# Optimization experiments

Measured on AMD Instinct MI355X. Metric: run time of the kernel, lower is better.

Reference implementation:

```python
import jax, jax.numpy as jnp
import numpy as np

N = 100000   # nodes
E = 640000   # edges
H = 8        # attention heads
C = 16       # hidden_channels (per-head out dim)
IN = 4       # in_channels
G = 64       # graphs in the batch
NE = 2       # num_experts
HC = H * C   # 128 = concat feature width
SLOPE = 0.2  # GATConv leaky_relu negative slope


def _p(k, shape):
    return 0.1 * jax.random.normal(k, shape, jnp.float32)


def setup_inputs() -> dict:
    key = jax.random.key(0)
    ks = jax.random.split(key, 32)
    inp = {
        "x": jax.random.normal(ks[0], (N, IN), jnp.float32),
        "edge_index": jax.random.randint(ks[1], (2, E), 0, N),
        "edge_attr": jax.random.normal(ks[2], (E, 1), jnp.float32),
        "batch": jnp.sort(jax.random.randint(ks[3], (N,), 0, G)),
    }
    i = 4
    for l, d in zip((1, 2, 3), (IN, HC, HC)):
        inp[f"w{l}"] = _p(ks[i], (d, HC)); i += 1      # node lin
        inp[f"as{l}"] = _p(ks[i], (H, C)); i += 1      # att_src
        inp[f"ad{l}"] = _p(ks[i], (H, C)); i += 1      # att_dst
        inp[f"we{l}"] = _p(ks[i], (1, HC)); i += 1     # lin_edge
        inp[f"ae{l}"] = _p(ks[i], (H, C)); i += 1      # att_edge
        inp[f"b{l}"] = jnp.zeros((HC,), jnp.float32)
    inp["fw1"] = _p(ks[i], (HC, 4 * C)); inp["fb1"] = jnp.zeros((4 * C,), jnp.float32)
    inp["fw2"] = _p(ks[i + 1], (4 * C, NE)); inp["fb2"] = jnp.zeros((NE,), jnp.float32)
    return inp


def gat_layer(x, src, dst, eattr, w, a_s, a_d, we, a_e, b):
    """PyG GATConv (concat=True, edge_dim=1): gather-attend-segment_softmax-scatter."""
    n = x.shape[0]
    h = (x @ w).reshape(n, H, C)                       # [N,H,C]
    alpha_src = jnp.sum(h * a_s, axis=-1)              # [N,H]
    alpha_dst = jnp.sum(h * a_d, axis=-1)              # [N,H]
    ef = (eattr @ we).reshape(-1, H, C)                # [E,H,C]
    alpha_e = jnp.sum(ef * a_e, axis=-1)               # [E,H]
    alpha = jax.nn.leaky_relu(alpha_src[src] + alpha_dst[dst] + alpha_e, SLOPE)
    # segment softmax over incoming edges of each dst node
    m = jax.lax.stop_gradient(jax.ops.segment_max(alpha, dst, num_segments=n))
    m = jnp.where(jnp.isfinite(m), m, 0.0)
    ex = jnp.exp(alpha - m[dst])
    den = jax.ops.segment_sum(ex, dst, num_segments=n)
    alpha = ex / (den[dst] + 1e-16)
    out = jax.ops.segment_sum(h[src] * alpha[:, :, None], dst, num_segments=n)
    return out.reshape(n, HC) + b


def add_self_loops_mean(src, dst, eattr, n):
    """add_self_loops(fill_value='mean'): self-loop attr = mean of incoming edge attrs."""
    cnt = jax.ops.segment_sum(jnp.ones(src.shape, eattr.dtype), dst, num_segments=n)
    loop = jax.ops.segment_sum(eattr, dst, num_segments=n) / jnp.maximum(cnt, 1.0)[:, None]
    idx = jnp.arange(n, dtype=src.dtype)
    return (jnp.concatenate([src, idx]), jnp.concatenate([dst, idx]),
            jnp.concatenate([eattr, loop], axis=0))


def reference(x, edge_index, edge_attr, batch,
              w1, as1, ad1, we1, ae1, b1,
              w2, as2, ad2, we2, ae2, b2,
              w3, as3, ad3, we3, ae3, b3,
              fw1, fb1, fw2, fb2):
    src, dst = edge_index[0], edge_index[1]
    # conv1: add_self_loops=False
    h = jax.nn.relu(gat_layer(x, src, dst, edge_attr, w1, as1, ad1, we1, ae1, b1))
    # conv2/conv3: default add_self_loops=True with fill_value='mean'
    s2, d2, e2 = add_self_loops_mean(src, dst, edge_attr, x.shape[0])
    h = jax.nn.relu(gat_layer(h, s2, d2, e2, w2, as2, ad2, we2, ae2, b2))
    h = jax.nn.relu(gat_layer(h, s2, d2, e2, w3, as3, ad3, we3, ae3, b3))
    # global mean pool over `batch`
    gsum = jax.ops.segment_sum(h, batch, num_segments=G)
    cnt = jax.ops.segment_sum(jnp.ones((h.shape[0],), h.dtype), batch, num_segments=G)
    emb = gsum / jnp.maximum(cnt, 1.0)[:, None]
    gh = jax.nn.relu(emb @ fw1 + fb1)
    return gh @ fw2 + fb2
```

## Files before the change

### kernel.cpp

```cpp
#include <hip/hip_runtime.h>
#include <hip/hip_bf16.h>
#include <math.h>

#define NHEAD 8
#define CDIM 16
#define HCDIM 128
#define NGRAPH 64
#define WEXT 144
#define SWPAD 136

typedef __attribute__((ext_vector_type(8))) short short8;
typedef __attribute__((ext_vector_type(4))) float f32x4;
typedef __attribute__((ext_vector_type(2))) float f32x2;

static __device__ __forceinline__ unsigned short f2bf(float f) {
    unsigned u = __float_as_uint(f);
    unsigned r = (u + 0x7FFF + ((u >> 16) & 1)) >> 16;
    return (unsigned short)r;
}
static __device__ __forceinline__ float bf2f(unsigned short s) {
    return __uint_as_float(((unsigned)s) << 16);
}
static __device__ __forceinline__ f32x2 bfpair(unsigned u) {
    return (f32x2){ __uint_as_float(u << 16), __uint_as_float(u & 0xffff0000u) };
}


__global__ void setup0(int* __restrict__ deg,
                       float* __restrict__ gsum,
                       const float* __restrict__ w2, const float* __restrict__ w3,
                       unsigned short* __restrict__ wt2, unsigned short* __restrict__ wt3,
                       const float* __restrict__ we1, const float* __restrict__ ae1,
                       const float* __restrict__ we2, const float* __restrict__ ae2,
                       const float* __restrict__ we3, const float* __restrict__ ae3,
                       float* __restrict__ kc,
                       const float* __restrict__ as2, const float* __restrict__ ad2,
                       const float* __restrict__ as3, const float* __restrict__ ad3,
                       const float* __restrict__ w1,
                       const float* __restrict__ as1, const float* __restrict__ ad1,
                       float* __restrict__ wastab, float* __restrict__ wadtab,
                       const int* __restrict__ batch, int* __restrict__ gstart, int n) {
    int i = blockIdx.x * 256 + threadIdx.x;
    if (i < n) deg[i] = 0;
    if (i < NGRAPH * HCDIM) gsum[i] = 0.f;
    if (i < WEXT * HCDIM) {
        int nn = i >> 7, k = i & 127;
        float v2, v3;
        if (nn < HCDIM) {
            v2 = w2[k * HCDIM + nn];
            v3 = w3[k * HCDIM + nn];
        } else if (nn < HCDIM + NHEAD) {
            int h = nn - HCDIM;
            float s2 = 0.f, s3 = 0.f;
#pragma unroll
            for (int c = 0; c < CDIM; ++c) {
                s2 += w2[k * HCDIM + h * CDIM + c] * as2[h * CDIM + c];
                s3 += w3[k * HCDIM + h * CDIM + c] * as3[h * CDIM + c];
            }
            v2 = s2; v3 = s3;
        } else {
            int h = nn - HCDIM - NHEAD;
            float s2 = 0.f, s3 = 0.f;
#pragma unroll
            for (int c = 0; c < CDIM; ++c) {
                s2 += w2[k * HCDIM + h * CDIM + c] * ad2[h * CDIM + c];
                s3 += w3[k * HCDIM + h * CDIM + c] * ad3[h * CDIM + c];
            }
            v2 = s2; v3 = s3;
        }
        wt2[nn * HCDIM + k] = f2bf(v2);
        wt3[nn * HCDIM + k] = f2bf(v3);
    }
    if (i < 24) {
        int l = i >> 3, h = i & 7;
        const float* we = (l == 0) ? we1 : ((l == 1) ? we2 : we3);
        const float* ae = (l == 0) ? ae1 : ((l == 1) ? ae2 : ae3);
        float s = 0.f;
        for (int c = 0; c < CDIM; ++c) s += we[h * CDIM + c] * ae[h * CDIM + c];
        kc[i] = s;
    }
    if (i >= 18560 && i <= 18560 + NGRAPH) {
        int g = i - 18560;
        int lo = 0, hi = n;
        while (lo < hi) {
            int mid = (lo + hi) >> 1;
            if (batch[mid] < g) lo = mid + 1; else hi = mid;
        }
        gstart[g] = lo;
    }
    if (i >= 18700 && i < 18732) {
        int t = i - 18700;
        int k = t >> 3, h = t & 7;
        float ss = 0.f, sd = 0.f;
#pragma unroll
        for (int c = 0; c < CDIM; ++c) {
            ss += w1[k * HCDIM + h * CDIM + c] * as1[h * CDIM + c];
            sd += w1[k * HCDIM + h * CDIM + c] * ad1[h * CDIM + c];
        }
        wastab[t] = ss;
        wadtab[t] = sd;
    }
}

__global__ void count_deg(const int* __restrict__ dst, int* __restrict__ deg,
                          int* __restrict__ erank, int E) {
    int e = blockIdx.x * 256 + threadIdx.x;
    if (e >= E) return;
    erank[e] = atomicAdd(&deg[dst[e]], 1);
}

__global__ __launch_bounds__(512) void block_sum(const int* __restrict__ deg,
                                                 int* __restrict__ bsum, int n) {
    __shared__ int s[512];
    int i = blockIdx.x * 512 + threadIdx.x;
    s[threadIdx.x] = (i < n) ? deg[i] : 0;
    __syncthreads();
    for (int off = 256; off > 0; off >>= 1) {
        if (threadIdx.x < off) s[threadIdx.x] += s[threadIdx.x + off];
        __syncthreads();
    }
    if (threadIdx.x == 0) bsum[blockIdx.x] = s[0];
}

__global__ __launch_bounds__(512) void scan_final2(const int* __restrict__ deg,
                                                   const int* __restrict__ bsum, int nb,
                                                   int* __restrict__ eoff, int n) {
    __shared__ int ls[512];
    __shared__ int s[512];
    const int t = threadIdx.x;
    ls[t] = (t < nb) ? bsum[t] : 0;
    int i = blockIdx.x * 512 + t;
    s[t] = (i < n) ? deg[i] : 0;
    __syncthreads();
    for (int off = 1; off < 512; off <<= 1) {
        int a1 = (t >= off) ? ls[t - off] : 0;
        int a2 = (t >= off) ? s[t - off] : 0;
        __syncthreads();
        ls[t] += a1; s[t] += a2;
        __syncthreads();
    }
    int base = (blockIdx.x > 0) ? ls[blockIdx.x - 1] : 0;
    if (i < n) eoff[i + 1] = base + s[t];
    if (i == 0) eoff[0] = 0;
}

__global__ void scatter_edges(const int* __restrict__ src, const int* __restrict__ dst,
                              const float* __restrict__ eattr,
                              const int* __restrict__ eoff,
                              const int* __restrict__ erank,
                              int2* __restrict__ epack, int E) {
    int e = blockIdx.x * 256 + threadIdx.x;
    if (e >= E) return;
    int p = eoff[dst[e]] + erank[e];
    epack[p] = make_int2(src[e], __float_as_int(eattr[e]));
}


__global__ __launch_bounds__(256) void gat_aggregate1(
    const float* __restrict__ x,
    const int2*  __restrict__ epack,
    const int*   __restrict__ eoff,
    const float* __restrict__ w1,
    const float* __restrict__ wastab,
    const float* __restrict__ wadtab,
    const float* __restrict__ kc,
    const float* __restrict__ bias,
    unsigned short* __restrict__ outbf,
    int n) {
    const int lane = threadIdx.x & 63;
    const int l16 = lane & 15;
    int nid = ((blockIdx.x * 256 + threadIdx.x) >> 6) * 4 + (lane >> 4);
    if (nid >= n) return;
    const int h = l16 >> 1;
    const int c0 = l16 * 8;

    float was0 = wastab[0 * NHEAD + h], was1_ = wastab[1 * NHEAD + h];
    float was2 = wastab[2 * NHEAD + h], was3 = wastab[3 * NHEAD + h];
    float wad0 = wadtab[0 * NHEAD + h], wad1_ = wadtab[1 * NHEAD + h];
    float wad2 = wadtab[2 * NHEAD + h], wad3 = wadtab[3 * NHEAD + h];

    f32x4 xd = *(const f32x4*)(x + (((unsigned)nid) << 2));
    const float adst_h = xd[0] * wad0 + xd[1] * wad1_ + xd[2] * wad2 + xd[3] * wad3;
    const float k_h = kc[h];
    const int e0 = eoff[nid], e1 = eoff[nid + 1];

    float den = 0.f;
    f32x4 acc4 = (f32x4){0.f, 0.f, 0.f, 0.f};

    if (e0 < e1) {
        int2 ep[4];
#pragma unroll
        for (int j = 0; j < 4; ++j) {
            int idx = e0 + j; idx = (idx < e1) ? idx : (e1 - 1);
            ep[j] = epack[idx];
        }
        for (int base = e0; base < e1; base += 4) {
            int2 epn[4];
#pragma unroll
            for (int j = 0; j < 4; ++j) {
                int idx = base + 4 + j; idx = (idx < e1) ? idx : (e1 - 1);
                epn[j] = epack[idx];
            }
            f32x4 xs[4];
#pragma unroll
            for (int j = 0; j < 4; ++j)
                xs[j] = *(const f32x4*)(x + (((unsigned)ep[j].x) << 2));
#pragma unroll
            for (int j = 0; j < 4; ++j) {
                bool valid = (base + j < e1);
                float as_e = xs[j][0] * was0 + xs[j][1] * was1_ +
                             xs[j][2] * was2 + xs[j][3] * was3;
                float a = as_e + adst_h + __int_as_float(ep[j].y) * k_h;
                a = (a > 0.f) ? a : 0.2f * a;
                float w = valid ? __expf(a) : 0.f;
                den += w;
                acc4 += xs[j] * w;
            }
#pragma unroll
            for (int j = 0; j < 4; ++j) ep[j] = epn[j];
        }
    }

    float inv = 1.f / (den + 1e-16f);
    short8 o;
#pragma unroll
    for (int c = 0; c < 8; ++c) {
        float oc = acc4[0] * w1[0 * HCDIM + c0 + c] + acc4[1] * w1[1 * HCDIM + c0 + c] +
                   acc4[2] * w1[2 * HCDIM + c0 + c] + acc4[3] * w1[3 * HCDIM + c0 + c];
        oc = fmaxf(oc * inv + bias[c0 + c], 0.f);
        o[c] = (short)f2bf(oc);
    }
    *(short8*)(outbf + (long)nid * HCDIM + c0) = o;
}


__global__ __launch_bounds__(256) void gemm_mfma(const unsigned short* __restrict__ A,
                                                 const unsigned short* __restrict__ Wt,
                                                 unsigned short* __restrict__ Ybf,
                                                 float* __restrict__ adstn, int n) {
    __shared__ unsigned short sW[WEXT][SWPAD];
    for (int i = threadIdx.x; i < WEXT * 16; i += 256) {
        int r = i >> 4, c = (i & 15) << 3;
        *(short8*)&sW[r][c] = *(const short8*)(Wt + r * HCDIM + c);
    }
    __syncthreads();

    const int wave = threadIdx.x >> 6;
    const int lane = threadIdx.x & 63;
    const int quad = lane >> 4;
    const int l16  = lane & 15;
    const int rowbase = (blockIdx.x * 8 + wave * 2) * 16;

    f32x4 acc[2][9];
#pragma unroll
    for (int r = 0; r < 2; ++r)
#pragma unroll
        for (int t = 0; t < 9; ++t) acc[r][t] = (f32x4){0.f, 0.f, 0.f, 0.f};

#pragma unroll
    for (int kb = 0; kb < HCDIM; kb += 32) {
        short8 a[2];
#pragma unroll
        for (int r = 0; r < 2; ++r) {
            int row = rowbase + r * 16 + l16;
            row = (row < n) ? row : (n - 1);
            a[r] = *(const short8*)(A + (long)row * HCDIM + kb + quad * 8);
        }
#pragma unroll
        for (int nt = 0; nt < 9; ++nt) {
            short8 b = *(const short8*)(&sW[nt * 16 + l16][kb + quad * 8]);
#pragma unroll
            for (int r = 0; r < 2; ++r)
                acc[r][nt] = __builtin_amdgcn_mfma_f32_16x16x32_bf16(a[r], b, acc[r][nt], 0, 0, 0);
        }
    }

#pragma unroll
    for (int r = 0; r < 2; ++r) {
#pragma unroll
        for (int reg = 0; reg < 4; ++reg) {
            int row = rowbase + r * 16 + quad * 4 + reg;
            if (row < n) {
                unsigned short* yp = Ybf + (long)row * HCDIM + l16;
#pragma unroll
                for (int nt = 0; nt < 8; ++nt) yp[nt * 16] = f2bf(acc[r][nt][reg]);
                if (l16 >= 8) adstn[row * NHEAD + (l16 - 8)] = acc[r][8][reg];
            }
        }
    }
}


__global__ __launch_bounds__(256) void gat_aggregate(
    const unsigned short* __restrict__ hlin,
    const float* __restrict__ adst,
    const float* __restrict__ asw,
    const int2*  __restrict__ epack,
    const int*   __restrict__ eoff,
    const float* __restrict__ kc,
    const float* __restrict__ bias,
    unsigned short* __restrict__ out,
    int n, int use_loop) {
    const int lane = threadIdx.x & 63;
    const int l16 = lane & 15;
    int nid = ((blockIdx.x * 256 + threadIdx.x) >> 6) * 4 + (lane >> 4);
    if (nid >= n) return;
    const int h = l16 >> 1;
    const int c0 = l16 * 8;

    const float* asrow = asw + h * CDIM + (l16 & 1) * 8;
    const f32x2 wp0 = *(const f32x2*)(asrow + 0);
    const f32x2 wp1 = *(const f32x2*)(asrow + 2);
    const f32x2 wp2 = *(const f32x2*)(asrow + 4);
    const f32x2 wp3 = *(const f32x2*)(asrow + 6);

    const float adst_h = adst[nid * NHEAD + h];
    const float k_h = kc[h];
    const int e0 = eoff[nid], e1 = eoff[nid + 1];

    float den = 0.f, sume = 0.f;
    f32x2 acc[4];
#pragma unroll
    for (int p = 0; p < 4; ++p) acc[p] = (f32x2){0.f, 0.f};

    if (e0 < e1) {
        int2 ep[4];
#pragma unroll
        for (int j = 0; j < 4; ++j) {
            int idx = e0 + j; idx = (idx < e1) ? idx : (e1 - 1);
            ep[j] = epack[idx];
        }
        for (int base = e0; base < e1; base += 4) {
            int2 epn[4];
#pragma unroll
            for (int j = 0; j < 4; ++j) {
                int idx = base + 4 + j; idx = (idx < e1) ? idx : (e1 - 1);
                epn[j] = epack[idx];
            }
            uint4 hv[4];
#pragma unroll
            for (int j = 0; j < 4; ++j)
                hv[j] = *(const uint4*)(hlin + (((unsigned)ep[j].x) << 7) + c0);
#pragma unroll
            for (int j = 0; j < 4; ++j) {
                bool valid = (base + j < e1);
                f32x2 p0 = bfpair(hv[j].x), p1 = bfpair(hv[j].y);
                f32x2 p2 = bfpair(hv[j].z), p3 = bfpair(hv[j].w);
                f32x2 ds = p0 * wp0 + p1 * wp1 + p2 * wp2 + p3 * wp3;
                float part = ds[0] + ds[1];
                float as_e = part + __shfl_xor(part, 1, 64);
                float ea = __int_as_float(ep[j].y);
                float a = as_e + adst_h + ea * k_h;
                a = (a > 0.f) ? a : 0.2f * a;
                float w = valid ? __expf(a) : 0.f;
                sume += valid ? ea : 0.f;
                den += w;
                acc[0] += p0 * w;
                acc[1] += p1 * w;
                acc[2] += p2 * w;
                acc[3] += p3 * w;
            }
#pragma unroll
            for (int j = 0; j < 4; ++j) ep[j] = epn[j];
        }
    }

    if (use_loop) {
        float fl = sume / fmaxf((float)(e1 - e0), 1.f);
        uint4 hv = *(const uint4*)(hlin + (((unsigned)nid) << 7) + c0);
        f32x2 p0 = bfpair(hv.x), p1 = bfpair(hv.y);
        f32x2 p2 = bfpair(hv.z), p3 = bfpair(hv.w);
        f32x2 ds = p0 * wp0 + p1 * wp1 + p2 * wp2 + p3 * wp3;
        float part = ds[0] + ds[1];
        float as_self = part + __shfl_xor(part, 1, 64);
        float a = as_self + adst_h + fl * k_h;
        a = (a > 0.f) ? a : 0.2f * a;
        float w = __expf(a);
        den += w;
        acc[0] += p0 * w;
        acc[1] += p1 * w;
        acc[2] += p2 * w;
        acc[3] += p3 * w;
    }

    float inv = 1.f / (den + 1e-16f);
    short8 o;
#pragma unroll
    for (int c = 0; c < 8; ++c) {
        float oc = fmaxf(acc[c >> 1][c & 1] * inv + bias[c0 + c], 0.f);
        o[c] = (short)f2bf(oc);
    }
    *(short8*)(out + (long)nid * HCDIM + c0) = o;
}


__global__ __launch_bounds__(128) void pool_seg(const unsigned short* __restrict__ H,
                                                const int* __restrict__ gstart,
                                                float* __restrict__ gsum) {
    const int c = threadIdx.x;
    const int g = blockIdx.x >> 3;
    const int chunk = blockIdx.x & 7;
    int s0 = gstart[g], s1 = gstart[g + 1];
    int len = s1 - s0;
    if (len <= 0) return;
    int cl = (len + 7) >> 3;
    int i0 = s0 + chunk * cl;
    int i1 = min(i0 + cl, s1);
    if (i0 >= i1) return;
    float acc = 0.f;
    int i = i0;
    for (; i + 4 <= i1; i += 4) {
        float v0 = bf2f(H[(long)i * HCDIM + c]);
        float v1 = bf2f(H[(long)(i + 1) * HCDIM + c]);
        float v2 = bf2f(H[(long)(i + 2) * HCDIM + c]);
        float v3 = bf2f(H[(long)(i + 3) * HCDIM + c]);
        acc += (v0 + v1) + (v2 + v3);
    }
    for (; i < i1; ++i) acc += bf2f(H[(long)i * HCDIM + c]);
    atomicAdd(&gsum[g * HCDIM + c], acc);
}

__global__ __launch_bounds__(64) void mlp_kernel(const float* __restrict__ gsum,
                                                 const int* __restrict__ gstart,
                                                 const float* __restrict__ fw1,
                                                 const float* __restrict__ fb1,
                                                 const float* __restrict__ fw2,
                                                 const float* __restrict__ fb2,
                                                 float* __restrict__ out) {
    const int g = blockIdx.x;
    const int j = threadIdx.x;
    __shared__ float emb[HCDIM];
    __shared__ float gh[64];
    int cnt = gstart[g + 1] - gstart[g];
    float invc = 1.f / fmaxf((float)cnt, 1.f);
    emb[j] = gsum[g * HCDIM + j] * invc;
    emb[j + 64] = gsum[g * HCDIM + 64 + j] * invc;
    __syncthreads();
    float a = fb1[j];
    for (int k = 0; k < HCDIM; ++k) a += emb[k] * fw1[k * 64 + j];
    gh[j] = fmaxf(a, 0.f);
    __syncthreads();
    if (j < 2) {
        float o = fb2[j];
        for (int k = 0; k < 64; ++k) o += gh[k] * fw2[k * 2 + j];
        out[g * 2 + j] = o;
    }
}


extern "C" void kernel_launch(void* const* d_in, const int* in_sizes, int n_in,
                              void* d_out, int out_size, void* d_ws, size_t ws_size,
                              hipStream_t stream) {
    const float* x     = (const float*)d_in[0];
    const int*   eidx  = (const int*)d_in[1];
    const float* eattr = (const float*)d_in[2];
    const int*   batch = (const int*)d_in[3];
    const float* w1  = (const float*)d_in[4];
    const float* as1 = (const float*)d_in[5];
    const float* ad1 = (const float*)d_in[6];
    const float* we1 = (const float*)d_in[7];
    const float* ae1 = (const float*)d_in[8];
    const float* b1  = (const float*)d_in[9];
    const float* w2  = (const float*)d_in[10];
    const float* as2 = (const float*)d_in[11];
    const float* ad2 = (const float*)d_in[12];
    const float* we2 = (const float*)d_in[13];
    const float* ae2 = (const float*)d_in[14];
    const float* b2  = (const float*)d_in[15];
    const float* w3  = (const float*)d_in[16];
    const float* as3 = (const float*)d_in[17];
    const float* ad3 = (const float*)d_in[18];
    const float* we3 = (const float*)d_in[19];
    const float* ae3 = (const float*)d_in[20];
    const float* b3  = (const float*)d_in[21];
    const float* fw1 = (const float*)d_in[22];
    const float* fb1 = (const float*)d_in[23];
    const float* fw2 = (const float*)d_in[24];
    const float* fb2 = (const float*)d_in[25];

    const int N = in_sizes[3];
    const int E = in_sizes[2];
    const int* src = eidx;
    const int* dst = eidx + E;

    char* p = (char*)d_ws;
    auto alloc = [&](size_t bytes) {
        void* r = (void*)p;
        p += (bytes + 255) & ~(size_t)255;
        return r;
    };
    unsigned short* Abf = (unsigned short*)alloc((size_t)N * HCDIM * 2);
    unsigned short* Bbf = (unsigned short*)alloc((size_t)N * HCDIM * 2);
    float* adstA  = (float*)alloc((size_t)N * NHEAD * 4);
    float* adstB  = (float*)alloc((size_t)N * NHEAD * 4);
    int*   deg    = (int*)alloc((size_t)N * 4);
    int*   eoff   = (int*)alloc((size_t)(N + 1) * 4);
    int*   erank  = (int*)alloc((size_t)E * 4);
    int2*  epack  = (int2*)alloc((size_t)E * 8);
    int*   bsum   = (int*)alloc(((size_t)(N + 511) / 512) * 4);
    float* kc     = (float*)alloc(24 * 4);
    int*   gstart = (int*)alloc((NGRAPH + 1) * 4);
    float* gsum   = (float*)alloc(NGRAPH * HCDIM * 4);
    float* wastab = (float*)alloc(32 * 4);
    float* wadtab = (float*)alloc(32 * 4);
    unsigned short* wt2 = (unsigned short*)alloc(WEXT * HCDIM * 2);
    unsigned short* wt3 = (unsigned short*)alloc(WEXT * HCDIM * 2);

    const int NB = (N + 255) / 256;
    const int NB512 = (N + 511) / 512;
    const int EB = (E + 255) / 256;
    const int AGG_BLOCKS = (((N + 3) / 4) * 64 + 255) / 256;
    const int GEMM_BLOCKS = (N + 127) / 128;

    setup0<<<NB, 256, 0, stream>>>(deg, gsum,
                                   w2, w3, wt2, wt3,
                                   we1, ae1, we2, ae2, we3, ae3, kc,
                                   as2, ad2, as3, ad3,
                                   w1, as1, ad1, wastab, wadtab,
                                   batch, gstart, N);
    count_deg<<<EB, 256, 0, stream>>>(dst, deg, erank, E);
    block_sum<<<NB512, 512, 0, stream>>>(deg, bsum, N);
    scan_final2<<<NB512, 512, 0, stream>>>(deg, bsum, NB512, eoff, N);
    scatter_edges<<<EB, 256, 0, stream>>>(src, dst, eattr, eoff, erank, epack, E);

    gat_aggregate1<<<AGG_BLOCKS, 256, 0, stream>>>(x, epack, eoff, w1, wastab, wadtab,
                                                   kc + 0, b1, Bbf, N);
    gemm_mfma<<<GEMM_BLOCKS, 256, 0, stream>>>(Bbf, wt2, Abf, adstB, N);
    gat_aggregate<<<AGG_BLOCKS, 256, 0, stream>>>(Abf, adstB, as2, epack, eoff,
                                                  kc + 8, b2, Bbf, N, 1);
    gemm_mfma<<<GEMM_BLOCKS, 256, 0, stream>>>(Bbf, wt3, Abf, adstA, N);
    gat_aggregate<<<AGG_BLOCKS, 256, 0, stream>>>(Abf, adstA, as3, epack, eoff,
                                                  kc + 16, b3, Bbf, N, 1);

    pool_seg<<<NGRAPH * 8, 128, 0, stream>>>(Bbf, gstart, gsum);
    mlp_kernel<<<NGRAPH, 64, 0, stream>>>(gsum, gstart, fw1, fb1, fw2, fb2, (float*)d_out);
}
```

Measured before the change: 319.6 us.

## Fuse GAT aggregation with next-layer MFMA GEMM and pooling; single-pass lookback scan

Each aggregation kernel now writes its 64-node tile of outputs into shared memory and runs the next layer's bf16 MFMA projection in the same block. This removes the intermediate global round-trip and the separate GEMM launches. The last aggregation accumulates the global mean-pool sums directly, using a block-level shared reduction when the tile belongs to a single graph. The two-kernel prefix scan is replaced by a decoupled lookback scan with spin-waiting on per-block flags. The trade-offs are: the weight matrix is read from global memory per MFMA instead of being staged in LDS, the edge prefetch pipelining is dropped, and the lookback scan depends on forward progress of earlier blocks.

```diff
diff --git a/kernel.cpp b/kernel.cpp
--- a/kernel.cpp
+++ b/kernel.cpp
@@ -7,7 +7,7 @@
 #define HCDIM 128
 #define NGRAPH 64
 #define WEXT 144
-#define SWPAD 136
+#define SAPAD 136
 
 typedef __attribute__((ext_vector_type(8))) short short8;
 typedef __attribute__((ext_vector_type(4))) float f32x4;
@@ -39,7 +39,8 @@
                        const float* __restrict__ w1,
                        const float* __restrict__ as1, const float* __restrict__ ad1,
                        float* __restrict__ wastab, float* __restrict__ wadtab,
-                       const int* __restrict__ batch, int* __restrict__ gstart, int n) {
+                       const int* __restrict__ batch, int* __restrict__ gstart,
+                       int* __restrict__ bflag, int n) {
     int i = blockIdx.x * 256 + threadIdx.x;
     if (i < n) deg[i] = 0;
     if (i < NGRAPH * HCDIM) gsum[i] = 0.f;
@@ -100,6 +101,7 @@
         wastab[t] = ss;
         wadtab[t] = sd;
     }
+    if (i >= 19000 && i < 19256) bflag[i - 19000] = 0;
 }
 
 __global__ void count_deg(const int* __restrict__ dst, int* __restrict__ deg,
@@ -109,37 +111,35 @@
     erank[e] = atomicAdd(&deg[dst[e]], 1);
 }
 
-__global__ __launch_bounds__(512) void block_sum(const int* __restrict__ deg,
-                                                 int* __restrict__ bsum, int n) {
+__global__ __launch_bounds__(512) void scan_lookback(const int* __restrict__ deg,
+                                                     int* __restrict__ bflag,
+                                                     int* __restrict__ eoff, int n) {
     __shared__ int s[512];
-    int i = blockIdx.x * 512 + threadIdx.x;
-    s[threadIdx.x] = (i < n) ? deg[i] : 0;
-    __syncthreads();
-    for (int off = 256; off > 0; off >>= 1) {
-        if (threadIdx.x < off) s[threadIdx.x] += s[threadIdx.x + off];
-        __syncthreads();
-    }
-    if (threadIdx.x == 0) bsum[blockIdx.x] = s[0];
-}
-
-__global__ __launch_bounds__(512) void scan_final2(const int* __restrict__ deg,
-                                                   const int* __restrict__ bsum, int nb,
-                                                   int* __restrict__ eoff, int n) {
     __shared__ int ls[512];
-    __shared__ int s[512];
     const int t = threadIdx.x;
-    ls[t] = (t < nb) ? bsum[t] : 0;
-    int i = blockIdx.x * 512 + t;
+    const int b = blockIdx.x;
+    int i = b * 512 + t;
     s[t] = (i < n) ? deg[i] : 0;
     __syncthreads();
     for (int off = 1; off < 512; off <<= 1) {
-        int a1 = (t >= off) ? ls[t - off] : 0;
-        int a2 = (t >= off) ? s[t - off] : 0;
+        int a = (t >= off) ? s[t - off] : 0;
         __syncthreads();
-        ls[t] += a1; s[t] += a2;
+        s[t] += a;
         __syncthreads();
     }
-    int base = (blockIdx.x > 0) ? ls[blockIdx.x - 1] : 0;
+    if (t == 0) atomicExch(&bflag[b], s[511] + 1);
+    ls[t] = 0;
+    if (t < b) {
+        int v;
+        do { v = atomicAdd(&bflag[t], 0); } while (v == 0);
+        ls[t] = v - 1;
+    }
+    __syncthreads();
+    for (int off = 256; off > 0; off >>= 1) {
+        if (t < off) ls[t] += ls[t + off];
+        __syncthreads();
+    }
+    int base = ls[0];
     if (i < n) eoff[i + 1] = base + s[t];
     if (i == 0) eoff[0] = 0;
 }
@@ -156,7 +156,7 @@
 }
 
 
-__global__ __launch_bounds__(256) void gat_aggregate1(
+__global__ __launch_bounds__(256, 4) void fused_l1(
     const float* __restrict__ x,
     const int2*  __restrict__ epack,
     const int*   __restrict__ eoff,
@@ -165,41 +165,39 @@
     const float* __restrict__ wadtab,
     const float* __restrict__ kc,
     const float* __restrict__ bias,
-    unsigned short* __restrict__ outbf,
+    const unsigned short* __restrict__ Wt,
+    unsigned short* __restrict__ Ybf,
+    float* __restrict__ adstn,
     int n) {
-    const int lane = threadIdx.x & 63;
-    const int l16 = lane & 15;
-    int nid = ((blockIdx.x * 256 + threadIdx.x) >> 6) * 4 + (lane >> 4);
-    if (nid >= n) return;
+    __shared__ unsigned short sA[64][SAPAD];
+    const int tid = threadIdx.x;
+    const int gi = tid >> 4;
+    const int l16 = tid & 15;
     const int h = l16 >> 1;
     const int c0 = l16 * 8;
+    const int nb = blockIdx.x * 64;
 
     float was0 = wastab[0 * NHEAD + h], was1_ = wastab[1 * NHEAD + h];
     float was2 = wastab[2 * NHEAD + h], was3 = wastab[3 * NHEAD + h];
     float wad0 = wadtab[0 * NHEAD + h], wad1_ = wadtab[1 * NHEAD + h];
     float wad2 = wadtab[2 * NHEAD + h], wad3 = wadtab[3 * NHEAD + h];
-
-    f32x4 xd = *(const f32x4*)(x + (((unsigned)nid) << 2));
-    const float adst_h = xd[0] * wad0 + xd[1] * wad1_ + xd[2] * wad2 + xd[3] * wad3;
     const float k_h = kc[h];
-    const int e0 = eoff[nid], e1 = eoff[nid + 1];
-
-    float den = 0.f;
-    f32x4 acc4 = (f32x4){0.f, 0.f, 0.f, 0.f};
-
-    if (e0 < e1) {
-        int2 ep[4];
-#pragma unroll
-        for (int j = 0; j < 4; ++j) {
-            int idx = e0 + j; idx = (idx < e1) ? idx : (e1 - 1);
-            ep[j] = epack[idx];
-        }
+
+    for (int s = 0; s < 4; ++s) {
+        int lr = (gi << 2) + s;
+        int nid = nb + lr;
+        if (nid >= n) continue;
+        f32x4 xd = *(const f32x4*)(x + (((unsigned)nid) << 2));
+        const float adst_h = xd[0] * wad0 + xd[1] * wad1_ + xd[2] * wad2 + xd[3] * wad3;
+        const int e0 = eoff[nid], e1 = eoff[nid + 1];
+        float den = 0.f;
+        f32x4 acc4 = (f32x4){0.f, 0.f, 0.f, 0.f};
         for (int base = e0; base < e1; base += 4) {
-            int2 epn[4];
+            int2 ep[4];
 #pragma unroll
             for (int j = 0; j < 4; ++j) {
-                int idx = base + 4 + j; idx = (idx < e1) ? idx : (e1 - 1);
-                epn[j] = epack[idx];
+                int idx = base + j; idx = (idx < e1) ? idx : (e1 - 1);
+                ep[j] = epack[idx];
             }
             f32x4 xs[4];
 #pragma unroll
@@ -216,82 +214,49 @@
                 den += w;
                 acc4 += xs[j] * w;
             }
-#pragma unroll
-            for (int j = 0; j < 4; ++j) ep[j] = epn[j];
-        }
-    }
-
-    float inv = 1.f / (den + 1e-16f);
-    short8 o;
-#pragma unroll
-    for (int c = 0; c < 8; ++c) {
-        float oc = acc4[0] * w1[0 * HCDIM + c0 + c] + acc4[1] * w1[1 * HCDIM + c0 + c] +
-                   acc4[2] * w1[2 * HCDIM + c0 + c] + acc4[3] * w1[3 * HCDIM + c0 + c];
-        oc = fmaxf(oc * inv + bias[c0 + c], 0.f);
-        o[c] = (short)f2bf(oc);
-    }
-    *(short8*)(outbf + (long)nid * HCDIM + c0) = o;
-}
-
-
-__global__ __launch_bounds__(256) void gemm_mfma(const unsigned short* __restrict__ A,
-                                                 const unsigned short* __restrict__ Wt,
-                                                 unsigned short* __restrict__ Ybf,
-                                                 float* __restrict__ adstn, int n) {
-    __shared__ unsigned short sW[WEXT][SWPAD];
-    for (int i = threadIdx.x; i < WEXT * 16; i += 256) {
-        int r = i >> 4, c = (i & 15) << 3;
-        *(short8*)&sW[r][c] = *(const short8*)(Wt + r * HCDIM + c);
+        }
+        float inv = 1.f / (den + 1e-16f);
+        short8 o;
+#pragma unroll
+        for (int c = 0; c < 8; ++c) {
+            float oc = acc4[0] * w1[0 * HCDIM + c0 + c] + acc4[1] * w1[1 * HCDIM + c0 + c] +
+                       acc4[2] * w1[2 * HCDIM + c0 + c] + acc4[3] * w1[3 * HCDIM + c0 + c];
+            oc = fmaxf(oc * inv + bias[c0 + c], 0.f);
+            o[c] = (short)f2bf(oc);
+        }
+        *(short8*)&sA[lr][c0] = o;
     }
     __syncthreads();
 
-    const int wave = threadIdx.x >> 6;
-    const int lane = threadIdx.x & 63;
+    const int wave = tid >> 6;
+    const int lane = tid & 63;
     const int quad = lane >> 4;
-    const int l16  = lane & 15;
-    const int rowbase = (blockIdx.x * 8 + wave * 2) * 16;
-
-    f32x4 acc[2][9];
-#pragma unroll
-    for (int r = 0; r < 2; ++r)
-#pragma unroll
-        for (int t = 0; t < 9; ++t) acc[r][t] = (f32x4){0.f, 0.f, 0.f, 0.f};
-
+    const int l16g = lane & 15;
+    f32x4 acc[9];
+#pragma unroll
+    for (int t = 0; t < 9; ++t) acc[t] = (f32x4){0.f, 0.f, 0.f, 0.f};
 #pragma unroll
     for (int kb = 0; kb < HCDIM; kb += 32) {
-        short8 a[2];
-#pragma unroll
-        for (int r = 0; r < 2; ++r) {
-            int row = rowbase + r * 16 + l16;
-            row = (row < n) ? row : (n - 1);
-            a[r] = *(const short8*)(A + (long)row * HCDIM + kb + quad * 8);
-        }
+        short8 a = *(const short8*)&sA[wave * 16 + l16g][kb + quad * 8];
 #pragma unroll
         for (int nt = 0; nt < 9; ++nt) {
-            short8 b = *(const short8*)(&sW[nt * 16 + l16][kb + quad * 8]);
-#pragma unroll
-            for (int r = 0; r < 2; ++r)
-                acc[r][nt] = __builtin_amdgcn_mfma_f32_16x16x32_bf16(a[r], b, acc[r][nt], 0, 0, 0);
-        }
-    }
-
-#pragma unroll
-    for (int r = 0; r < 2; ++r) {
-#pragma unroll
-        for (int reg = 0; reg < 4; ++reg) {
-            int row = rowbase + r * 16 + quad * 4 + reg;
-            if (row < n) {
-                unsigned short* yp = Ybf + (long)row * HCDIM + l16;
-#pragma unroll
-                for (int nt = 0; nt < 8; ++nt) yp[nt * 16] = f2bf(acc[r][nt][reg]);
-                if (l16 >= 8) adstn[row * NHEAD + (l16 - 8)] = acc[r][8][reg];
-            }
-        }
-    }
-}
-
-
-__global__ __launch_bounds__(256) void gat_aggregate(
+            short8 b = *(const short8*)(Wt + (nt * 16 + l16g) * HCDIM + kb + quad * 8);
+            acc[nt] = __builtin_amdgcn_mfma_f32_16x16x32_bf16(a, b, acc[nt], 0, 0, 0);
+        }
+    }
+#pragma unroll
+    for (int reg = 0; reg < 4; ++reg) {
+        int row = nb + wave * 16 + quad * 4 + reg;
+        if (row < n) {
+            unsigned short* yp = Ybf + (long)row * HCDIM + l16g;
+#pragma unroll
+            for (int nt = 0; nt < 8; ++nt) yp[nt * 16] = f2bf(acc[nt][reg]);
+            if (l16g >= 8) adstn[row * NHEAD + (l16g - 8)] = acc[8][reg];
+        }
+    }
+}
+
+__global__ __launch_bounds__(256, 4) void fused_l23(
     const unsigned short* __restrict__ hlin,
     const float* __restrict__ adst,
     const float* __restrict__ asw,
@@ -299,43 +264,41 @@
     const int*   __restrict__ eoff,
     const float* __restrict__ kc,
     const float* __restrict__ bias,
-    unsigned short* __restrict__ out,
-    int n, int use_loop) {
-    const int lane = threadIdx.x & 63;
-    const int l16 = lane & 15;
-    int nid = ((blockIdx.x * 256 + threadIdx.x) >> 6) * 4 + (lane >> 4);
-    if (nid >= n) return;
+    const unsigned short* __restrict__ Wt,
+    unsigned short* __restrict__ Ybf,
+    float* __restrict__ adstn,
+    int n) {
+    __shared__ unsigned short sA[64][SAPAD];
+    const int tid = threadIdx.x;
+    const int gi = tid >> 4;
+    const int l16 = tid & 15;
     const int h = l16 >> 1;
     const int c0 = l16 * 8;
+    const int nb = blockIdx.x * 64;
 
     const float* asrow = asw + h * CDIM + (l16 & 1) * 8;
     const f32x2 wp0 = *(const f32x2*)(asrow + 0);
     const f32x2 wp1 = *(const f32x2*)(asrow + 2);
     const f32x2 wp2 = *(const f32x2*)(asrow + 4);
     const f32x2 wp3 = *(const f32x2*)(asrow + 6);
-
-    const float adst_h = adst[nid * NHEAD + h];
     const float k_h = kc[h];
-    const int e0 = eoff[nid], e1 = eoff[nid + 1];
-
-    float den = 0.f, sume = 0.f;
-    f32x2 acc[4];
-#pragma unroll
-    for (int p = 0; p < 4; ++p) acc[p] = (f32x2){0.f, 0.f};
-
-    if (e0 < e1) {
-        int2 ep[4];
-#pragma unroll
-        for (int j = 0; j < 4; ++j) {
-            int idx = e0 + j; idx = (idx < e1) ? idx : (e1 - 1);
-            ep[j] = epack[idx];
-        }
+
+    for (int s = 0; s < 4; ++s) {
+        int lr = (gi << 2) + s;
+        int nid = nb + lr;
+        if (nid >= n) continue;
+        const float adst_h = adst[nid * NHEAD + h];
+        const int e0 = eoff[nid], e1 = eoff[nid + 1];
+        float den = 0.f, sume = 0.f;
+        f32x2 acc[4];
+#pragma unroll
+        for (int p = 0; p < 4; ++p) acc[p] = (f32x2){0.f, 0.f};
         for (int base = e0; base < e1; base += 4) {
-            int2 epn[4];
+            int2 ep[4];
 #pragma unroll
             for (int j = 0; j < 4; ++j) {
-                int idx = base + 4 + j; idx = (idx < e1) ? idx : (e1 - 1);
-                epn[j] = epack[idx];
+                int idx = base + j; idx = (idx < e1) ? idx : (e1 - 1);
+                ep[j] = epack[idx];
             }
             uint4 hv[4];
 #pragma unroll
@@ -360,65 +323,183 @@
                 acc[2] += p2 * w;
                 acc[3] += p3 * w;
             }
-#pragma unroll
-            for (int j = 0; j < 4; ++j) ep[j] = epn[j];
-        }
-    }
-
-    if (use_loop) {
-        float fl = sume / fmaxf((float)(e1 - e0), 1.f);
-        uint4 hv = *(const uint4*)(hlin + (((unsigned)nid) << 7) + c0);
-        f32x2 p0 = bfpair(hv.x), p1 = bfpair(hv.y);
-        f32x2 p2 = bfpair(hv.z), p3 = bfpair(hv.w);
-        f32x2 ds = p0 * wp0 + p1 * wp1 + p2 * wp2 + p3 * wp3;
-        float part = ds[0] + ds[1];
-        float as_self = part + __shfl_xor(part, 1, 64);
-        float a = as_self + adst_h + fl * k_h;
-        a = (a > 0.f) ? a : 0.2f * a;
-        float w = __expf(a);
-        den += w;
-        acc[0] += p0 * w;
-        acc[1] += p1 * w;
-        acc[2] += p2 * w;
-        acc[3] += p3 * w;
-    }
-
-    float inv = 1.f / (den + 1e-16f);
-    short8 o;
-#pragma unroll
-    for (int c = 0; c < 8; ++c) {
-        float oc = fmaxf(acc[c >> 1][c & 1] * inv + bias[c0 + c], 0.f);
-        o[c] = (short)f2bf(oc);
-    }
-    *(short8*)(out + (long)nid * HCDIM + c0) = o;
-}
-
-
-__global__ __launch_bounds__(128) void pool_seg(const unsigned short* __restrict__ H,
-                                                const int* __restrict__ gstart,
-                                                float* __restrict__ gsum) {
-    const int c = threadIdx.x;
-    const int g = blockIdx.x >> 3;
-    const int chunk = blockIdx.x & 7;
-    int s0 = gstart[g], s1 = gstart[g + 1];
-    int len = s1 - s0;
-    if (len <= 0) return;
-    int cl = (len + 7) >> 3;
-    int i0 = s0 + chunk * cl;
-    int i1 = min(i0 + cl, s1);
-    if (i0 >= i1) return;
-    float acc = 0.f;
-    int i = i0;
-    for (; i + 4 <= i1; i += 4) {
-        float v0 = bf2f(H[(long)i * HCDIM + c]);
-        float v1 = bf2f(H[(long)(i + 1) * HCDIM + c]);
-        float v2 = bf2f(H[(long)(i + 2) * HCDIM + c]);
-        float v3 = bf2f(H[(long)(i + 3) * HCDIM + c]);
-        acc += (v0 + v1) + (v2 + v3);
-    }
-    for (; i < i1; ++i) acc += bf2f(H[(long)i * HCDIM + c]);
-    atomicAdd(&gsum[g * HCDIM + c], acc);
-}
+        }
+        {
+            float fl = sume / fmaxf((float)(e1 - e0), 1.f);
+            uint4 hv = *(const uint4*)(hlin + (((unsigned)nid) << 7) + c0);
+            f32x2 p0 = bfpair(hv.x), p1 = bfpair(hv.y);
+            f32x2 p2 = bfpair(hv.z), p3 = bfpair(hv.w);
+            f32x2 ds = p0 * wp0 + p1 * wp1 + p2 * wp2 + p3 * wp3;
+            float part = ds[0] + ds[1];
+            float as_self = part + __shfl_xor(part, 1, 64);
+            float a = as_self + adst_h + fl * k_h;
+            a = (a > 0.f) ? a : 0.2f * a;
+            float w = __expf(a);
+            den += w;
+            acc[0] += p0 * w;
+            acc[1] += p1 * w;
+            acc[2] += p2 * w;
+            acc[3] += p3 * w;
+        }
+        float inv = 1.f / (den + 1e-16f);
+        short8 o;
+#pragma unroll
+        for (int c = 0; c < 8; ++c) {
+            float oc = fmaxf(acc[c >> 1][c & 1] * inv + bias[c0 + c], 0.f);
+            o[c] = (short)f2bf(oc);
+        }
+        *(short8*)&sA[lr][c0] = o;
+    }
+    __syncthreads();
+
+    const int wave = tid >> 6;
+    const int lane = tid & 63;
+    const int quad = lane >> 4;
+    const int l16g = lane & 15;
+    f32x4 acc[9];
+#pragma unroll
+    for (int t = 0; t < 9; ++t) acc[t] = (f32x4){0.f, 0.f, 0.f, 0.f};
+#pragma unroll
+    for (int kb = 0; kb < HCDIM; kb += 32) {
+        short8 a = *(const short8*)&sA[wave * 16 + l16g][kb + quad * 8];
+#pragma unroll
+        for (int nt = 0; nt < 9; ++nt) {
+            short8 b = *(const short8*)(Wt + (nt * 16 + l16g) * HCDIM + kb + quad * 8);
+            acc[nt] = __builtin_amdgcn_mfma_f32_16x16x32_bf16(a, b, acc[nt], 0, 0, 0);
+        }
+    }
+#pragma unroll
+    for (int reg = 0; reg < 4; ++reg) {
+        int row = nb + wave * 16 + quad * 4 + reg;
+        if (row < n) {
+            unsigned short* yp = Ybf + (long)row * HCDIM + l16g;
+#pragma unroll
+            for (int nt = 0; nt < 8; ++nt) yp[nt * 16] = f2bf(acc[nt][reg]);
+            if (l16g >= 8) adstn[row * NHEAD + (l16g - 8)] = acc[8][reg];
+        }
+    }
+}
+
+__global__ __launch_bounds__(256) void fused_pool(
+    const unsigned short* __restrict__ hlin,
+    const float* __restrict__ adst,
+    const float* __restrict__ asw,
+    const int2*  __restrict__ epack,
+    const int*   __restrict__ eoff,
+    const float* __restrict__ kc,
+    const float* __restrict__ bias,
+    const int*   __restrict__ batch,
+    float* __restrict__ gsum,
+    int n) {
+    __shared__ float gacc[HCDIM];
+    const int tid = threadIdx.x;
+    const int gi = tid >> 4;
+    const int l16 = tid & 15;
+    const int h = l16 >> 1;
+    const int c0 = l16 * 8;
+    const int nb = blockIdx.x * 64;
+
+    if (tid < HCDIM) gacc[tid] = 0.f;
+    __syncthreads();
+
+    const int g0 = batch[(nb < n) ? nb : (n - 1)];
+    const int gL = batch[((nb + 63) < n) ? (nb + 63) : (n - 1)];
+    const bool uni = (g0 == gL);
+
+    const float* asrow = asw + h * CDIM + (l16 & 1) * 8;
+    const f32x2 wp0 = *(const f32x2*)(asrow + 0);
+    const f32x2 wp1 = *(const f32x2*)(asrow + 2);
+    const f32x2 wp2 = *(const f32x2*)(asrow + 4);
+    const f32x2 wp3 = *(const f32x2*)(asrow + 6);
+    const float k_h = kc[h];
+
+    float rsum[8];
+#pragma unroll
+    for (int c = 0; c < 8; ++c) rsum[c] = 0.f;
+
+    for (int s = 0; s < 4; ++s) {
+        int lr = (gi << 2) + s;
+        int nid = nb + lr;
+        if (nid >= n) continue;
+        const float adst_h = adst[nid * NHEAD + h];
+        const int e0 = eoff[nid], e1 = eoff[nid + 1];
+        float den = 0.f, sume = 0.f;
+        f32x2 acc[4];
+#pragma unroll
+        for (int p = 0; p < 4; ++p) acc[p] = (f32x2){0.f, 0.f};
+        for (int base = e0; base < e1; base += 4) {
+            int2 ep[4];
+#pragma unroll
+            for (int j = 0; j < 4; ++j) {
+                int idx = base + j; idx = (idx < e1) ? idx : (e1 - 1);
+                ep[j] = epack[idx];
+            }
+            uint4 hv[4];
+#pragma unroll
+            for (int j = 0; j < 4; ++j)
+                hv[j] = *(const uint4*)(hlin + (((unsigned)ep[j].x) << 7) + c0);
+#pragma unroll
+            for (int j = 0; j < 4; ++j) {
+                bool valid = (base + j < e1);
+                f32x2 p0 = bfpair(hv[j].x), p1 = bfpair(hv[j].y);
+                f32x2 p2 = bfpair(hv[j].z), p3 = bfpair(hv[j].w);
+                f32x2 ds = p0 * wp0 + p1 * wp1 + p2 * wp2 + p3 * wp3;
+                float part = ds[0] + ds[1];
+                float as_e = part + __shfl_xor(part, 1, 64);
+                float ea = __int_as_float(ep[j].y);
+                float a = as_e + adst_h + ea * k_h;
+                a = (a > 0.f) ? a : 0.2f * a;
+                float w = valid ? __expf(a) : 0.f;
+                sume += valid ? ea : 0.f;
+                den += w;
+                acc[0] += p0 * w;
+                acc[1] += p1 * w;
+                acc[2] += p2 * w;
+                acc[3] += p3 * w;
+            }
+        }
+        {
+            float fl = sume / fmaxf((float)(e1 - e0), 1.f);
+            uint4 hv = *(const uint4*)(hlin + (((unsigned)nid) << 7) + c0);
+            f32x2 p0 = bfpair(hv.x), p1 = bfpair(hv.y);
+            f32x2 p2 = bfpair(hv.z), p3 = bfpair(hv.w);
+            f32x2 ds = p0 * wp0 + p1 * wp1 + p2 * wp2 + p3 * wp3;
+            float part = ds[0] + ds[1];
+            float as_self = part + __shfl_xor(part, 1, 64);
+            float a = as_self + adst_h + fl * k_h;
+            a = (a > 0.f) ? a : 0.2f * a;
+            float w = __expf(a);
+            den += w;
+            acc[0] += p0 * w;
+            acc[1] += p1 * w;
+            acc[2] += p2 * w;
+            acc[3] += p3 * w;
+        }
+        float inv = 1.f / (den + 1e-16f);
+        if (uni) {
+#pragma unroll
+            for (int c = 0; c < 8; ++c) {
+                float oc = fmaxf(acc[c >> 1][c & 1] * inv + bias[c0 + c], 0.f);
+                rsum[c] += bf2f(f2bf(oc));
+            }
+        } else {
+            int g = batch[nid];
+#pragma unroll
+            for (int c = 0; c < 8; ++c) {
+                float oc = fmaxf(acc[c >> 1][c & 1] * inv + bias[c0 + c], 0.f);
+                atomicAdd(&gsum[g * HCDIM + c0 + c], bf2f(f2bf(oc)));
+            }
+        }
+    }
+
+    if (uni) {
+#pragma unroll
+        for (int c = 0; c < 8; ++c) atomicAdd(&gacc[c0 + c], rsum[c]);
+        __syncthreads();
+        if (tid < HCDIM) atomicAdd(&gsum[g0 * HCDIM + tid], gacc[tid]);
+    }
+}
+
 
 __global__ __launch_bounds__(64) void mlp_kernel(const float* __restrict__ gsum,
                                                  const int* __restrict__ gstart,
@@ -490,14 +571,14 @@
         return r;
     };
     unsigned short* Abf = (unsigned short*)alloc((size_t)N * HCDIM * 2);
-    unsigned short* Bbf = (unsigned short*)alloc((size_t)N * HCDIM * 2);
+    unsigned short* Cbf = (unsigned short*)alloc((size_t)N * HCDIM * 2);
     float* adstA  = (float*)alloc((size_t)N * NHEAD * 4);
     float* adstB  = (float*)alloc((size_t)N * NHEAD * 4);
     int*   deg    = (int*)alloc((size_t)N * 4);
     int*   eoff   = (int*)alloc((size_t)(N + 1) * 4);
     int*   erank  = (int*)alloc((size_t)E * 4);
     int2*  epack  = (int2*)alloc((size_t)E * 8);
-    int*   bsum   = (int*)alloc(((size_t)(N + 511) / 512) * 4);
+    int*   bflag  = (int*)alloc(256 * 4);
     float* kc     = (float*)alloc(24 * 4);
     int*   gstart = (int*)alloc((NGRAPH + 1) * 4);
     float* gsum   = (float*)alloc(NGRAPH * HCDIM * 4);
@@ -509,29 +590,23 @@
     const int NB = (N + 255) / 256;
     const int NB512 = (N + 511) / 512;
     const int EB = (E + 255) / 256;
-    const int AGG_BLOCKS = (((N + 3) / 4) * 64 + 255) / 256;
-    const int GEMM_BLOCKS = (N + 127) / 128;
+    const int FUSED_BLOCKS = (N + 63) / 64;
 
     setup0<<<NB, 256, 0, stream>>>(deg, gsum,
                                    w2, w3, wt2, wt3,
                                    we1, ae1, we2, ae2, we3, ae3, kc,
                                    as2, ad2, as3, ad3,
                                    w1, as1, ad1, wastab, wadtab,
-                                   batch, gstart, N);
+                                   batch, gstart, bflag, N);
     count_deg<<<EB, 256, 0, stream>>>(dst, deg, erank, E);
-    block_sum<<<NB512, 512, 0, stream>>>(deg, bsum, N);
-    scan_final2<<<NB512, 512, 0, stream>>>(deg, bsum, NB512, eoff, N);
+    scan_lookback<<<NB512, 512, 0, stream>>>(deg, bflag, eoff, N);
     scatter_edges<<<EB, 256, 0, stream>>>(src, dst, eattr, eoff, erank, epack, E);
 
-    gat_aggregate1<<<AGG_BLOCKS, 256, 0, stream>>>(x, epack, eoff, w1, wastab, wadtab,
-                                                   kc + 0, b1, Bbf, N);
-    gemm_mfma<<<GEMM_BLOCKS, 256, 0, stream>>>(Bbf, wt2, Abf, adstB, N);
-    gat_aggregate<<<AGG_BLOCKS, 256, 0, stream>>>(Abf, adstB, as2, epack, eoff,
-                                                  kc + 8, b2, Bbf, N, 1);
-    gemm_mfma<<<GEMM_BLOCKS, 256, 0, stream>>>(Bbf, wt3, Abf, adstA, N);
-    gat_aggregate<<<AGG_BLOCKS, 256, 0, stream>>>(Abf, adstA, as3, epack, eoff,
-                                                  kc + 16, b3, Bbf, N, 1);
-
-    pool_seg<<<NGRAPH * 8, 128, 0, stream>>>(Bbf, gstart, gsum);
+    fused_l1<<<FUSED_BLOCKS, 256, 0, stream>>>(x, epack, eoff, w1, wastab, wadtab,
+                                               kc + 0, b1, wt2, Abf, adstB, N);
+    fused_l23<<<FUSED_BLOCKS, 256, 0, stream>>>(Abf, adstB, as2, epack, eoff,
+                                                kc + 8, b2, wt3, Cbf, adstA, N);
+    fused_pool<<<FUSED_BLOCKS, 256, 0, stream>>>(Cbf, adstA, as3, epack, eoff,
+                                                 kc + 16, b3, batch, gsum, N);
     mlp_kernel<<<NGRAPH, 64, 0, stream>>>(gsum, gstart, fw1, fb1, fw2, fb2, (float*)d_out);
 }
```

After: 375.3 us. 1.17x slower.

## Sort nodes by degree within 1024-node tiles to balance aggregation wavefronts

Applied to the files above, without the earlier changes.

Adds a bitonic sort kernel that orders each tile of 1024 nodes by in-degree and writes a permutation. The three aggregation kernels map each 16-lane group to a node through this permutation, so the four nodes sharing a wavefront have similar edge counts and less lane divergence. The cost is an extra kernel launch, one more indirect load per node, and scattered output writes and edoff reads, which lose some locality.

```diff
diff --git a/kernel.cpp b/kernel.cpp
--- a/kernel.cpp
+++ b/kernel.cpp
@@ -109,6 +109,37 @@
     erank[e] = atomicAdd(&deg[dst[e]], 1);
 }
 
+__global__ __launch_bounds__(512) void sort_tile(const int* __restrict__ deg,
+                                                 int* __restrict__ perm, int n) {
+    __shared__ unsigned key[1024];
+    const int base = blockIdx.x << 10;
+    const int t = threadIdx.x;
+    for (int j = t; j < 1024; j += 512) {
+        int i = base + j;
+        unsigned d = (i < n) ? (unsigned)deg[i] : 0x1FFFFFu;
+        key[j] = (d << 11) | (unsigned)j;
+    }
+    __syncthreads();
+    for (int k = 2; k <= 1024; k <<= 1) {
+        for (int jj = k >> 1; jj > 0; jj >>= 1) {
+            for (int idx = t; idx < 1024; idx += 512) {
+                int ixj = idx ^ jj;
+                if (ixj > idx) {
+                    unsigned a = key[idx], b = key[ixj];
+                    bool asc = ((idx & k) == 0);
+                    bool sw = asc ? (a > b) : (a < b);
+                    if (sw) { key[idx] = b; key[ixj] = a; }
+                }
+            }
+            __syncthreads();
+        }
+    }
+    for (int j = t; j < 1024; j += 512) {
+        int i = base + j;
+        if (i < n) perm[i] = base + (int)(key[j] & 2047u);
+    }
+}
+
 __global__ __launch_bounds__(512) void block_sum(const int* __restrict__ deg,
                                                  int* __restrict__ bsum, int n) {
     __shared__ int s[512];
@@ -160,6 +191,7 @@
     const float* __restrict__ x,
     const int2*  __restrict__ epack,
     const int*   __restrict__ eoff,
+    const int*   __restrict__ perm,
     const float* __restrict__ w1,
     const float* __restrict__ wastab,
     const float* __restrict__ wadtab,
@@ -169,8 +201,9 @@
     int n) {
     const int lane = threadIdx.x & 63;
     const int l16 = lane & 15;
-    int nid = ((blockIdx.x * 256 + threadIdx.x) >> 6) * 4 + (lane >> 4);
-    if (nid >= n) return;
+    int lin = ((blockIdx.x * 256 + threadIdx.x) >> 6) * 4 + (lane >> 4);
+    if (lin >= n) return;
+    const int nid = perm[lin];
     const int h = l16 >> 1;
     const int c0 = l16 * 8;
 
@@ -297,14 +330,16 @@
     const float* __restrict__ asw,
     const int2*  __restrict__ epack,
     const int*   __restrict__ eoff,
+    const int*   __restrict__ perm,
     const float* __restrict__ kc,
     const float* __restrict__ bias,
     unsigned short* __restrict__ out,
     int n, int use_loop) {
     const int lane = threadIdx.x & 63;
     const int l16 = lane & 15;
-    int nid = ((blockIdx.x * 256 + threadIdx.x) >> 6) * 4 + (lane >> 4);
-    if (nid >= n) return;
+    int lin = ((blockIdx.x * 256 + threadIdx.x) >> 6) * 4 + (lane >> 4);
+    if (lin >= n) return;
+    const int nid = perm[lin];
     const int h = l16 >> 1;
     const int c0 = l16 * 8;
 
@@ -498,6 +533,7 @@
     int*   erank  = (int*)alloc((size_t)E * 4);
     int2*  epack  = (int2*)alloc((size_t)E * 8);
     int*   bsum   = (int*)alloc(((size_t)(N + 511) / 512) * 4);
+    int*   perm   = (int*)alloc((size_t)N * 4);
     float* kc     = (float*)alloc(24 * 4);
     int*   gstart = (int*)alloc((NGRAPH + 1) * 4);
     float* gsum   = (float*)alloc(NGRAPH * HCDIM * 4);
@@ -509,6 +545,7 @@
     const int NB = (N + 255) / 256;
     const int NB512 = (N + 511) / 512;
     const int EB = (E + 255) / 256;
+    const int NTILE = (N + 1023) / 1024;
     const int AGG_BLOCKS = (((N + 3) / 4) * 64 + 255) / 256;
     const int GEMM_BLOCKS = (N + 127) / 128;
 
@@ -519,17 +556,18 @@
                                    w1, as1, ad1, wastab, wadtab,
                                    batch, gstart, N);
     count_deg<<<EB, 256, 0, stream>>>(dst, deg, erank, E);
+    sort_tile<<<NTILE, 512, 0, stream>>>(deg, perm, N);
     block_sum<<<NB512, 512, 0, stream>>>(deg, bsum, N);
     scan_final2<<<NB512, 512, 0, stream>>>(deg, bsum, NB512, eoff, N);
     scatter_edges<<<EB, 256, 0, stream>>>(src, dst, eattr, eoff, erank, epack, E);
 
-    gat_aggregate1<<<AGG_BLOCKS, 256, 0, stream>>>(x, epack, eoff, w1, wastab, wadtab,
-                                                   kc + 0, b1, Bbf, N);
+    gat_aggregate1<<<AGG_BLOCKS, 256, 0, stream>>>(x, epack, eoff, perm, w1, wastab,
+                                                   wadtab, kc + 0, b1, Bbf, N);
     gemm_mfma<<<GEMM_BLOCKS, 256, 0, stream>>>(Bbf, wt2, Abf, adstB, N);
-    gat_aggregate<<<AGG_BLOCKS, 256, 0, stream>>>(Abf, adstB, as2, epack, eoff,
+    gat_aggregate<<<AGG_BLOCKS, 256, 0, stream>>>(Abf, adstB, as2, epack, eoff, perm,
                                                   kc + 8, b2, Bbf, N, 1);
     gemm_mfma<<<GEMM_BLOCKS, 256, 0, stream>>>(Bbf, wt3, Abf, adstA, N);
-    gat_aggregate<<<AGG_BLOCKS, 256, 0, stream>>>(Abf, adstA, as3, epack, eoff,
+    gat_aggregate<<<AGG_BLOCKS, 256, 0, stream>>>(Abf, adstA, as3, epack, eoff, perm,
                                                   kc + 16, b3, Bbf, N, 1);
 
     pool_seg<<<NGRAPH * 8, 128, 0, stream>>>(Bbf, gstart, gsum);
```

After: 347.4 us. 1.09x slower.
